# Performance work log

Hardware: AMD Instinct MI355X
Metric: run time of the kernel (lower is better)

Reference implementation:

```python
import jax, jax.numpy as jnp
import numpy as np

B_, L_, DM = 64, 2048, 12
DI, DS, DC, DTR = 24, 16, 4, 1  # d_inner=expand*d_model, d_state, d_conv, dt_rank=ceil(12/16)


def _ln(x, g, b, eps=1e-12):
    m = x.mean(-1, keepdims=True)
    v = ((x - m) ** 2).mean(-1, keepdims=True)
    return (x - m) / jnp.sqrt(v + eps) * g + b


def setup_inputs() -> dict:
    key = jax.random.key(0)
    ks = jax.random.split(key, 16)
    r = lambda k, s, sc=0.1: jax.random.normal(k, s, jnp.float32) * sc
    A = jnp.tile(jnp.arange(1, DS + 1, dtype=jnp.float32), (DI, 1))  # standard S4D-real init
    return {
        "x": jax.random.normal(ks[0], (B_, L_, DM), jnp.float32),
        "in_proj_w": r(ks[1], (2 * DI, DM)),
        "conv_w": r(ks[2], (DI, 1, DC)),
        "conv_b": r(ks[3], (DI,)),
        "x_proj_w": r(ks[4], (DTR + 2 * DS, DI)),
        "dt_w": r(ks[5], (DI, DTR)),
        "dt_b": r(ks[6], (DI,)),
        "A_log": jnp.log(A),
        "Dp": r(ks[7], (DI,)) + 1.0,
        "out_proj_w": r(ks[8], (DM, DI)),
        "ln1_g": jnp.ones(DM, jnp.float32), "ln1_b": jnp.zeros(DM, jnp.float32),
        "ffn_w1": r(ks[9], (4 * DM, DM)), "ffn_b1": jnp.zeros(4 * DM, jnp.float32),
        "ffn_w2": r(ks[10], (DM, 4 * DM)), "ffn_b2": jnp.zeros(DM, jnp.float32),
        "ffn_ln_g": jnp.ones(DM, jnp.float32), "ffn_ln_b": jnp.zeros(DM, jnp.float32),
        "cnn_w": r(ks[11], (DM, DM, 3)), "cnn_b": r(ks[12], (DM,)),
        "lin1_w": r(ks[13], (12, 24)), "lin1_b": jnp.zeros(12, jnp.float32),
        "lin2_w": r(ks[14], (20, 12)), "lin2_b": jnp.zeros(20, jnp.float32),
        "lin3_w": r(ks[15], (1, 20)), "lin3_b": jnp.zeros(1, jnp.float32),
    }


def reference(x, in_proj_w, conv_w, conv_b, x_proj_w, dt_w, dt_b, A_log, Dp,
              out_proj_w, ln1_g, ln1_b, ffn_w1, ffn_b1, ffn_w2, ffn_b2,
              ffn_ln_g, ffn_ln_b, cnn_w, cnn_b, lin1_w, lin1_b,
              lin2_w, lin2_b, lin3_w, lin3_b):
    Bsz = x.shape[0]
    # ---- Mamba block ----
    xz = jnp.einsum('bld,ed->ble', x, in_proj_w)            # [B,L,2*DI]
    xi, z = xz[..., :DI], xz[..., DI:]
    xc = jax.lax.conv_general_dilated(
        xi.transpose(0, 2, 1), conv_w, (1,), [(DC - 1, 0)],
        dimension_numbers=('NCH', 'OIH', 'NCH'), feature_group_count=DI)
    xi = jax.nn.silu(xc.transpose(0, 2, 1) + conv_b)        # causal depthwise conv + SiLU
    xdb = jnp.einsum('bld,ed->ble', xi, x_proj_w)           # [B,L,dt_rank+2*DS]
    dt, Bm, Cm = xdb[..., :DTR], xdb[..., DTR:DTR + DS], xdb[..., DTR + DS:]
    delta = jax.nn.softplus(jnp.einsum('blr,dr->bld', dt, dt_w) + dt_b)  # [B,L,DI]
    A = -jnp.exp(A_log)                                     # [DI,DS]
    dA = jnp.exp(delta[..., None] * A)                      # [B,L,DI,DS]
    dBx = delta[..., None] * Bm[:, :, None, :] * xi[..., None]

    def step(h, inp):
        a, bx, c = inp
        h = a * h + bx                                      # [B,DI,DS]
        return h, jnp.einsum('bdn,bn->bd', h, c)

    h0 = jnp.zeros((Bsz, DI, DS), x.dtype)
    _, ys = jax.lax.scan(step, h0, (dA.transpose(1, 0, 2, 3),
                                    dBx.transpose(1, 0, 2, 3),
                                    Cm.transpose(1, 0, 2)))
    y = ys.transpose(1, 0, 2) + xi * Dp                     # skip D*x
    y = y * jax.nn.silu(z)
    m_out = jnp.einsum('ble,de->bld', y, out_proj_w)        # [B,L,DM]
    h = _ln(m_out, ln1_g, ln1_b)                            # num_layers==1: no residual
    # ---- FeedForward (with residual + LN) ----
    ff = jax.nn.gelu(jnp.einsum('bld,ed->ble', h, ffn_w1) + ffn_b1, approximate=False)
    ff = jnp.einsum('ble,de->bld', ff, ffn_w2) + ffn_b2
    x_mamba = _ln(ff + h, ffn_ln_g, ffn_ln_b)
    # ---- FFT magnitude + Conv1d path (padding=1 to keep length L; see notes) ----
    xf = jnp.abs(jnp.fft.fft(x, axis=1)).astype(x.dtype)
    xcnn = jax.lax.conv_general_dilated(
        xf.transpose(0, 2, 1), cnn_w, (1,), [(1, 1)],
        dimension_numbers=('NCH', 'OIH', 'NCH')) + cnn_b[None, :, None]
    xcnn = xcnn.transpose(0, 2, 1)                          # [B,L,12]
    # ---- fusion head ----
    comb = jnp.concatenate([x_mamba, xcnn], axis=-1)        # [B,L,24]
    o = jax.nn.elu(jnp.einsum('ble,de->bld', comb, lin1_w) + lin1_b)
    o = jnp.einsum('bld,ed->ble', o, lin2_w) + lin2_b
    o = jnp.einsum('ble,oe->blo', o, lin3_w) + lin3_b       # [B,L,1]
    return jax.nn.sigmoid(o.mean(axis=1)).squeeze()          # [B]
```

## Files before the change

kernel.cpp:

```cpp
#include <hip/hip_runtime.h>
#include <math.h>

#define B_  64
#define L_  2048
#define DM  12
#define DI  24
#define DS  16
#define DC  4
#define DTR 1
#define T_  (B_ * L_)
#define NCHUNK 128
#define CHUNK  16


__device__ __forceinline__ float siluf(float v)  { return v / (1.0f + __expf(-v)); }
__device__ __forceinline__ float eluf(float v) { return v > 0.0f ? v : __expf(v) - 1.0f; }

__device__ __forceinline__ float fast_erff(float x) {
    const float ax = fabsf(x);
    const float t  = 1.0f / fmaf(0.3275911f, ax, 1.0f);
    float p = fmaf(1.061405429f, t, -1.453152027f);
    p = fmaf(p, t, 1.421413741f);
    p = fmaf(p, t, -0.284496736f);
    p = fmaf(p, t, 0.254829592f);
    p *= t;
    const float r = 1.0f - p * __expf(-ax * ax);
    return copysignf(r, x);
}
__device__ __forceinline__ float geluf(float v) {
    return 0.5f * v * (1.0f + fast_erff(v * 0.70710678118654752440f));
}

__global__ __launch_bounds__(256) void k_proj(
    const float* __restrict__ x, const float* __restrict__ w_in,
    const float* __restrict__ conv_w, const float* __restrict__ conv_b,
    const float* __restrict__ xproj_w,
    float* __restrict__ xi_out, float* __restrict__ zs_out,
    float* __restrict__ dt_out, float* __restrict__ Bm_out,
    float* __restrict__ Cm_out)
{
    __shared__ float s_xi[256 + 3][DI + 1];
    __shared__ float s_st[256 * DI];
    const int tid = threadIdx.x;
    const int b   = blockIdx.x >> 3;
    const int l0  = (blockIdx.x & 7) << 8;
    const int l   = l0 + tid;
    const int t   = b * L_ + l;
    const size_t t0 = (size_t)b * L_ + l0;

    float xv[DM];
    *(float4*)&xv[0] = *(const float4*)&x[t * DM + 0];
    *(float4*)&xv[4] = *(const float4*)&x[t * DM + 4];
    *(float4*)&xv[8] = *(const float4*)&x[t * DM + 8];

    float zsv[DI];
#pragma unroll
    for (int e = 0; e < DI; ++e) {
        float acc = 0.0f, accz = 0.0f;
#pragma unroll
        for (int d = 0; d < DM; ++d) {
            acc  += xv[d] * w_in[e * DM + d];
            accz += xv[d] * w_in[(DI + e) * DM + d];
        }
        s_xi[tid + 3][e] = acc;
        zsv[e] = siluf(accz);
    }
    if (tid < 3) {
        const int lh = l0 - 3 + tid;
        if (lh < 0) {
            for (int e = 0; e < DI; ++e) s_xi[tid][e] = 0.0f;
        } else {
            const int th = b * L_ + lh;
            float xh[DM];
            for (int d = 0; d < DM; ++d) xh[d] = x[th * DM + d];
            for (int e = 0; e < DI; ++e) {
                float acc = 0.0f;
                for (int d = 0; d < DM; ++d) acc += xh[d] * w_in[e * DM + d];
                s_xi[tid][e] = acc;
            }
        }
    }
#pragma unroll
    for (int e = 0; e < DI; ++e) s_st[tid * DI + e] = zsv[e];
    __syncthreads();
    {
        float4* g = (float4*)(zs_out + t0 * DI);
        const float4* s4 = (const float4*)s_st;
#pragma unroll
        for (int k = 0; k < 6; ++k) g[k * 256 + tid] = s4[k * 256 + tid];
    }

    float xi[DI];
#pragma unroll
    for (int dch = 0; dch < DI; ++dch) {
        float acc = conv_b[dch];
#pragma unroll
        for (int k = 0; k < DC; ++k) acc += s_xi[tid + k][dch] * conv_w[dch * DC + k];
        xi[dch] = siluf(acc);
    }
    float dt = 0.0f;
#pragma unroll
    for (int d = 0; d < DI; ++d) dt += xi[d] * xproj_w[d];
    dt_out[t] = dt;
    float Bv[DS], Cv[DS];
#pragma unroll
    for (int e = 0; e < DS; ++e) {
        float accB = 0.0f, accC = 0.0f;
#pragma unroll
        for (int d = 0; d < DI; ++d) {
            accB += xi[d] * xproj_w[(1 + e) * DI + d];
            accC += xi[d] * xproj_w[(1 + DS + e) * DI + d];
        }
        Bv[e] = accB;
        Cv[e] = accC;
    }

    __syncthreads();
#pragma unroll
    for (int e = 0; e < DI; ++e) s_st[tid * DI + e] = xi[e];
    __syncthreads();
    {
        float4* g = (float4*)(xi_out + t0 * DI);
        const float4* s4 = (const float4*)s_st;
#pragma unroll
        for (int k = 0; k < 6; ++k) g[k * 256 + tid] = s4[k * 256 + tid];
    }
    __syncthreads();
#pragma unroll
    for (int e = 0; e < DS; ++e) s_st[tid * DS + e] = Bv[e];
    __syncthreads();
    {
        float4* g = (float4*)(Bm_out + t0 * DS);
        const float4* s4 = (const float4*)s_st;
#pragma unroll
        for (int k = 0; k < 4; ++k) g[k * 256 + tid] = s4[k * 256 + tid];
    }
    __syncthreads();
#pragma unroll
    for (int e = 0; e < DS; ++e) s_st[tid * DS + e] = Cv[e];
    __syncthreads();
    {
        float4* g = (float4*)(Cm_out + t0 * DS);
        const float4* s4 = (const float4*)s_st;
#pragma unroll
        for (int k = 0; k < 4; ++k) g[k * 256 + tid] = s4[k * 256 + tid];
    }
}

__global__ __launch_bounds__(384) void k_scan1(
    const float* __restrict__ dt_in, const float* __restrict__ xi,
    const float* __restrict__ Bm, const float* __restrict__ A_log,
    const float* __restrict__ dt_w, const float* __restrict__ dt_b,
    float* __restrict__ Sd, float* __restrict__ H)
{
    const int tid = threadIdx.x;
    const int d   = tid % DI;
    const int cl  = tid / DI;
    const int b   = blockIdx.x >> 3;
    const int c   = ((blockIdx.x & 7) << 4) + cl;
    const int t0  = b * L_ + c * CHUNK;

    float An[DS];
#pragma unroll
    for (int j = 0; j < DS; ++j) An[j] = -__expf(A_log[d * DS + j]);
    const float dtw = dt_w[d], dtb = dt_b[d];

    float h[DS];
#pragma unroll
    for (int j = 0; j < DS; ++j) h[j] = 0.0f;
    float sumdel = 0.0f;

    const float*  pDt = dt_in + t0;
    const float*  pX  = xi + (size_t)t0 * DI + d;
    const float4* pB  = (const float4*)(Bm + (size_t)t0 * DS);

#pragma unroll 4
    for (int i = 0; i < CHUNK; ++i) {
        const float v = fmaf(pDt[i], dtw, dtb);
        const float e = __expf(v);
        const float delta = (v > 20.0f) ? v : __logf(1.0f + e);
        const float u = delta * pX[i * DI];
        sumdel += delta;
        const float4 B0 = pB[i * 4 + 0];
        const float4 B1 = pB[i * 4 + 1];
        const float4 B2 = pB[i * 4 + 2];
        const float4 B3 = pB[i * 4 + 3];
#pragma unroll
        for (int j = 0; j < DS; ++j) {
            const float a = __expf(delta * An[j]);
            h[j] = a * h[j] + u * ((j < 4) ? (&B0.x)[j] : (j < 8) ? (&B1.x)[j - 4]
                                   : (j < 12) ? (&B2.x)[j - 8] : (&B3.x)[j - 12]);
        }
    }
    const int cu = (b * DI + d) * NCHUNK + c;
    Sd[cu] = sumdel;
    float4* pH = (float4*)(H + (size_t)cu * DS);
    pH[0] = make_float4(h[0], h[1], h[2], h[3]);
    pH[1] = make_float4(h[4], h[5], h[6], h[7]);
    pH[2] = make_float4(h[8], h[9], h[10], h[11]);
    pH[3] = make_float4(h[12], h[13], h[14], h[15]);
}

__global__ __launch_bounds__(256) void k_scan2(
    const float* __restrict__ Sd, float* __restrict__ H,
    const float* __restrict__ A_log)
{
    const int idx  = blockIdx.x * 256 + threadIdx.x;
    const int n    = idx & 15;
    const int rest = idx >> 4;
    const int d    = rest % DI;
    const float An = -__expf(A_log[d * DS + n]);
    float Hc = 0.0f;
    const int base = rest * NCHUNK;
    for (int cg = 0; cg < NCHUNK / 8; ++cg) {
        float sd[8], hh[8];
#pragma unroll
        for (int k = 0; k < 8; ++k) {
            sd[k] = Sd[base + cg * 8 + k];
            hh[k] = H[(base + cg * 8 + k) * DS + n];
        }
        float aa[8];
#pragma unroll
        for (int k = 0; k < 8; ++k) aa[k] = __expf(An * sd[k]);
#pragma unroll
        for (int k = 0; k < 8; ++k) {
            H[(base + cg * 8 + k) * DS + n] = Hc;
            Hc = aa[k] * Hc + hh[k];
        }
    }
}

__global__ __launch_bounds__(384) void k_scan3(
    const float* __restrict__ dt_in, const float* __restrict__ xi,
    const float* __restrict__ Bm, const float* __restrict__ Cm,
    const float* __restrict__ zs, const float* __restrict__ Dp,
    const float* __restrict__ H0, const float* __restrict__ A_log,
    const float* __restrict__ dt_w, const float* __restrict__ dt_b,
    float* __restrict__ y_out)
{
    const int tid = threadIdx.x;
    const int d   = tid % DI;
    const int cl  = tid / DI;
    const int b   = blockIdx.x >> 3;
    const int c   = ((blockIdx.x & 7) << 4) + cl;
    const int t0  = b * L_ + c * CHUNK;

    float An[DS];
#pragma unroll
    for (int j = 0; j < DS; ++j) An[j] = -__expf(A_log[d * DS + j]);
    const float dtw = dt_w[d], dtb = dt_b[d];
    const float Dpd = Dp[d];

    const int cu = (b * DI + d) * NCHUNK + c;
    float h[DS];
    {
        const float4* pH0 = (const float4*)(H0 + (size_t)cu * DS);
        const float4 a0 = pH0[0], a1 = pH0[1], a2 = pH0[2], a3 = pH0[3];
        h[0]=a0.x; h[1]=a0.y; h[2]=a0.z; h[3]=a0.w;
        h[4]=a1.x; h[5]=a1.y; h[6]=a1.z; h[7]=a1.w;
        h[8]=a2.x; h[9]=a2.y; h[10]=a2.z; h[11]=a2.w;
        h[12]=a3.x; h[13]=a3.y; h[14]=a3.z; h[15]=a3.w;
    }

    const float*  pDt = dt_in + t0;
    const float*  pX  = xi + (size_t)t0 * DI + d;
    const float*  pZ  = zs + (size_t)t0 * DI + d;
    const float4* pB  = (const float4*)(Bm + (size_t)t0 * DS);
    const float4* pC  = (const float4*)(Cm + (size_t)t0 * DS);
    float*        pY  = y_out + (size_t)t0 * DI + d;

#pragma unroll 4
    for (int i = 0; i < CHUNK; ++i) {
        const float v = fmaf(pDt[i], dtw, dtb);
        const float e = __expf(v);
        const float delta = (v > 20.0f) ? v : __logf(1.0f + e);
        const float xiv = pX[i * DI];
        const float u = delta * xiv;
        const float4 B0 = pB[i * 4 + 0];
        const float4 B1 = pB[i * 4 + 1];
        const float4 B2 = pB[i * 4 + 2];
        const float4 B3 = pB[i * 4 + 3];
        const float4 C0 = pC[i * 4 + 0];
        const float4 C1 = pC[i * 4 + 1];
        const float4 C2 = pC[i * 4 + 2];
        const float4 C3 = pC[i * 4 + 3];
        float p = 0.0f;
#pragma unroll
        for (int j = 0; j < DS; ++j) {
            const float a = __expf(delta * An[j]);
            const float Bj = (j < 4) ? (&B0.x)[j] : (j < 8) ? (&B1.x)[j - 4]
                             : (j < 12) ? (&B2.x)[j - 8] : (&B3.x)[j - 12];
            const float Cj = (j < 4) ? (&C0.x)[j] : (j < 8) ? (&C1.x)[j - 4]
                             : (j < 12) ? (&C2.x)[j - 8] : (&C3.x)[j - 12];
            h[j] = a * h[j] + u * Bj;
            p += h[j] * Cj;
        }
        pY[i * DI] = (p + xiv * Dpd) * pZ[i * DI];
    }
}

__global__ __launch_bounds__(256) void k_fft(
    const float* __restrict__ x, float* __restrict__ xfT)
{
    __shared__ float re[2048], im[2048], twr[1024], twi[1024];
    const int tid = threadIdx.x;
    const int b   = blockIdx.x / (DM / 2);
    const int p   = blockIdx.x % (DM / 2);
    for (int j = tid; j < 1024; j += 256) {
        const float ang = -6.283185307179586f * (float)j * (1.0f / 2048.0f);
        float s, c;
        sincosf(ang, &s, &c);
        twr[j] = c; twi[j] = s;
    }
    for (int i = tid; i < 2048; i += 256) {
        const int r = (int)(__brev((unsigned)i) >> 21);
        const float2 v = *(const float2*)&x[(size_t)(b * L_ + i) * DM + 2 * p];
        re[r] = v.x;
        im[r] = v.y;
    }
    __syncthreads();
    for (int s = 1; s <= 11; ++s) {
        const int half  = 1 << (s - 1);
        const int tstep = 2048 >> s;
        for (int i = tid; i < 1024; i += 256) {
            const int j   = i & (half - 1);
            const int grp = i >> (s - 1);
            const int pos = (grp << s) + j;
            const float wr = twr[j * tstep], wi = twi[j * tstep];
            const float ar = re[pos + half], ai = im[pos + half];
            const float vr = wr * ar - wi * ai;
            const float vi = wr * ai + wi * ar;
            const float ur = re[pos], ui = im[pos];
            re[pos] = ur + vr;          im[pos] = ui + vi;
            re[pos + half] = ur - vr;   im[pos + half] = ui - vi;
        }
        __syncthreads();
    }
    float* row1 = xfT + (size_t)(b * DM + 2 * p) * L_;
    float* row2 = row1 + L_;
    for (int k = tid; k < 2048; k += 256) {
        const int nk = (2048 - k) & 2047;
        const float zr = re[k],  zi = im[k];
        const float qr = re[nk], qi = im[nk];
        const float e1r = zr + qr, e1i = zi - qi;
        const float e2r = zr - qr, e2i = zi + qi;
        row1[k] = 0.5f * sqrtf(e1r * e1r + e1i * e1i);
        row2[k] = 0.5f * sqrtf(e2r * e2r + e2i * e2i);
    }
}

__global__ __launch_bounds__(256, 2) void k_tail(
    const float* __restrict__ yg, const float* __restrict__ xfT,
    const float* __restrict__ out_w,
    const float* __restrict__ ln1_g, const float* __restrict__ ln1_b,
    const float* __restrict__ w1, const float* __restrict__ b1,
    const float* __restrict__ w2, const float* __restrict__ b2,
    const float* __restrict__ lng, const float* __restrict__ lnb,
    const float* __restrict__ cnn_w, const float* __restrict__ cnn_b,
    const float* __restrict__ l1w, const float* __restrict__ l1b,
    const float* __restrict__ l2w, const float* __restrict__ l2b,
    const float* __restrict__ l3w,
    float* __restrict__ part)
{
    __shared__ float sV[DM];
    __shared__ float sC0;
    __shared__ float sred[256];

    const int tid = threadIdx.x;
    const int b   = blockIdx.x >> 3;
    const int l   = ((blockIdx.x & 7) << 8) + tid;
    const int t   = b * L_ + l;

    float y[DI];
#pragma unroll
    for (int e = 0; e < DI; ++e) y[e] = yg[(size_t)t * DI + e];
    float xfm[DM], xf0[DM], xfp[DM];
#pragma unroll
    for (int i = 0; i < DM; ++i) {
        const float* row = xfT + (size_t)(b * DM + i) * L_;
        xfm[i] = (l == 0)      ? 0.0f : row[l - 1];
        xf0[i] = row[l];
        xfp[i] = (l == L_ - 1) ? 0.0f : row[l + 1];
    }

    if (tid < DM) {
        float acc = 0.0f;
#pragma unroll
        for (int e = 0; e < 20; ++e) acc += l3w[e] * l2w[e * DM + tid];
        sV[tid] = acc;
    }
    if (tid == DM) {
        float c = 0.0f;
#pragma unroll
        for (int e = 0; e < 20; ++e) c += l2b[e] * l3w[e];
        sC0 = c;
    }
    __syncthreads();

    float m[DM];
#pragma unroll
    for (int j = 0; j < DM; ++j) {
        float acc = 0.0f;
#pragma unroll
        for (int e = 0; e < DI; ++e) acc += y[e] * out_w[j * DI + e];
        m[j] = acc;
    }
    float mean = 0.0f;
#pragma unroll
    for (int j = 0; j < DM; ++j) mean += m[j];
    mean *= (1.0f / DM);
    float var = 0.0f;
#pragma unroll
    for (int j = 0; j < DM; ++j) { const float dv = m[j] - mean; var += dv * dv; }
    var *= (1.0f / DM);
    const float inv1 = rsqrtf(var + 1e-12f);
    float h[DM];
#pragma unroll
    for (int j = 0; j < DM; ++j) h[j] = (m[j] - mean) * inv1 * ln1_g[j] + ln1_b[j];

    float ff[4 * DM];
#pragma unroll
    for (int e = 0; e < 4 * DM; ++e) {
        float acc = b1[e];
#pragma unroll
        for (int j = 0; j < DM; ++j) acc += h[j] * w1[e * DM + j];
        ff[e] = geluf(acc);
    }
    float f2[DM];
#pragma unroll
    for (int j = 0; j < DM; ++j) {
        float acc = b2[j];
#pragma unroll
        for (int e = 0; e < 4 * DM; ++e) acc += ff[e] * w2[j * (4 * DM) + e];
        f2[j] = acc + h[j];
    }
    mean = 0.0f;
#pragma unroll
    for (int j = 0; j < DM; ++j) mean += f2[j];
    mean *= (1.0f / DM);
    var = 0.0f;
#pragma unroll
    for (int j = 0; j < DM; ++j) { const float dv = f2[j] - mean; var += dv * dv; }
    var *= (1.0f / DM);
    const float inv2 = rsqrtf(var + 1e-12f);
    float xm[DM];
#pragma unroll
    for (int j = 0; j < DM; ++j) xm[j] = (f2[j] - mean) * inv2 * lng[j] + lnb[j];

    float xc[DM];
#pragma unroll
    for (int o = 0; o < DM; ++o) {
        float acc = cnn_b[o];
#pragma unroll
        for (int i = 0; i < DM; ++i) {
            const int wb = (o * DM + i) * 3;
            acc += xfm[i] * cnn_w[wb] + xf0[i] * cnn_w[wb + 1] + xfp[i] * cnn_w[wb + 2];
        }
        xc[o] = acc;
    }

    float o3 = sC0;
#pragma unroll
    for (int d = 0; d < DM; ++d) {
        float acc = l1b[d];
#pragma unroll
        for (int e = 0; e < DM; ++e) acc += xm[e] * l1w[d * (2 * DM) + e];
#pragma unroll
        for (int e = 0; e < DM; ++e) acc += xc[e] * l1w[d * (2 * DM) + DM + e];
        o3 += eluf(acc) * sV[d];
    }

    sred[tid] = o3;
    __syncthreads();
    for (int s = 128; s > 0; s >>= 1) {
        if (tid < s) sred[tid] += sred[tid + s];
        __syncthreads();
    }
    if (tid == 0) part[blockIdx.x] = sred[0];
}

__global__ void k_final(const float* __restrict__ part, const float* __restrict__ l3b,
                        float* __restrict__ out)
{
    const int b = threadIdx.x;
    if (b < B_) {
        float s = 0.0f;
        for (int i = 0; i < 8; ++i) s += part[b * 8 + i];
        s = s * (1.0f / (float)L_) + l3b[0];
        out[b] = 1.0f / (1.0f + __expf(-s));
    }
}

extern "C" void kernel_launch(void* const* d_in, const int* in_sizes, int n_in,
                              void* d_out, int out_size, void* d_ws, size_t ws_size,
                              hipStream_t stream)
{
    const float* x        = (const float*)d_in[0];
    const float* in_w     = (const float*)d_in[1];
    const float* conv_w   = (const float*)d_in[2];
    const float* conv_b   = (const float*)d_in[3];
    const float* xproj_w  = (const float*)d_in[4];
    const float* dt_w     = (const float*)d_in[5];
    const float* dt_b     = (const float*)d_in[6];
    const float* A_log    = (const float*)d_in[7];
    const float* Dp       = (const float*)d_in[8];
    const float* out_w    = (const float*)d_in[9];
    const float* ln1_g    = (const float*)d_in[10];
    const float* ln1_b    = (const float*)d_in[11];
    const float* ffn_w1   = (const float*)d_in[12];
    const float* ffn_b1   = (const float*)d_in[13];
    const float* ffn_w2   = (const float*)d_in[14];
    const float* ffn_b2   = (const float*)d_in[15];
    const float* ffn_ln_g = (const float*)d_in[16];
    const float* ffn_ln_b = (const float*)d_in[17];
    const float* cnn_w    = (const float*)d_in[18];
    const float* cnn_b    = (const float*)d_in[19];
    const float* l1w      = (const float*)d_in[20];
    const float* l1b      = (const float*)d_in[21];
    const float* l2w      = (const float*)d_in[22];
    const float* l2b      = (const float*)d_in[23];
    const float* l3w      = (const float*)d_in[24];
    const float* l3b      = (const float*)d_in[25];
    float* out = (float*)d_out;

    float* ws = (float*)d_ws;
    const size_t nTDI = (size_t)T_ * DI;
    const size_t nTDS = (size_t)T_ * DS;
    const size_t nCH  = (size_t)B_ * DI * NCHUNK;
    float* w_xi   = ws;
    float* w_zs   = w_xi + nTDI;
    float* w_y    = w_zs + nTDI;
    float* w_dt   = w_y + nTDI;
    float* w_Bm   = w_dt + T_;
    float* w_Cm   = w_Bm + nTDS;
    float* w_Sd   = w_Cm + nTDS;
    float* w_H    = w_Sd + nCH;
    float* w_xf   = w_H + nCH * DS;
    float* w_part = w_xf + (size_t)B_ * DM * L_;

    k_proj<<<512, 256, 0, stream>>>(x, in_w, conv_w, conv_b, xproj_w,
                                    w_xi, w_zs, w_dt, w_Bm, w_Cm);
    k_scan1<<<B_ * (NCHUNK / 16), 384, 0, stream>>>(w_dt, w_xi, w_Bm, A_log,
                                                    dt_w, dt_b, w_Sd, w_H);
    k_scan2<<<96, 256, 0, stream>>>(w_Sd, w_H, A_log);
    k_fft<<<B_ * (DM / 2), 256, 0, stream>>>(x, w_xf);
    k_scan3<<<B_ * (NCHUNK / 16), 384, 0, stream>>>(w_dt, w_xi, w_Bm, w_Cm, w_zs, Dp,
                                                    w_H, A_log, dt_w, dt_b, w_y);
    k_tail<<<512, 256, 0, stream>>>(w_y, w_xf, out_w,
                                    ln1_g, ln1_b, ffn_w1, ffn_b1, ffn_w2, ffn_b2,
                                    ffn_ln_g, ffn_ln_b, cnn_w, cnn_b,
                                    l1w, l1b, l2w, l2b, l3w, w_part);
    k_final<<<1, 64, 0, stream>>>(w_part, l3b, out);
}
```

Measured before the change: 164.3 us.

## Fuse three-pass chunked scan into one kernel and merge FFT into projection

The three scan kernels (local chunk scan, serial carry propagation, rescan) become one kernel where each block owns one (batch, channel) pair and its 128 chunks. Carries are combined with a Hillis-Steele scan in shared memory, which drops the Sd/H global round trip and two launches. The FFT blocks are appended to the projection grid so both run in a single launch and can overlap. The trade-offs are block-wide syncs in the log-step scan, small 128-thread blocks, and a shared smem buffer sized for the larger of the two roles.

After: 293.9 us. +78.9%, slower.

```diff
diff --git a/kernel.cpp b/kernel.cpp
--- a/kernel.cpp
+++ b/kernel.cpp
@@ -31,149 +31,204 @@
     return 0.5f * v * (1.0f + fast_erff(v * 0.70710678118654752440f));
 }
 
-__global__ __launch_bounds__(256) void k_proj(
+__global__ __launch_bounds__(256) void k_proj_fft(
     const float* __restrict__ x, const float* __restrict__ w_in,
     const float* __restrict__ conv_w, const float* __restrict__ conv_b,
     const float* __restrict__ xproj_w,
     float* __restrict__ xi_out, float* __restrict__ zs_out,
     float* __restrict__ dt_out, float* __restrict__ Bm_out,
-    float* __restrict__ Cm_out)
+    float* __restrict__ Cm_out, float* __restrict__ xfT)
 {
-    __shared__ float s_xi[256 + 3][DI + 1];
-    __shared__ float s_st[256 * DI];
+    __shared__ float smem[12620];
     const int tid = threadIdx.x;
-    const int b   = blockIdx.x >> 3;
-    const int l0  = (blockIdx.x & 7) << 8;
-    const int l   = l0 + tid;
-    const int t   = b * L_ + l;
-    const size_t t0 = (size_t)b * L_ + l0;
-
-    float xv[DM];
-    *(float4*)&xv[0] = *(const float4*)&x[t * DM + 0];
-    *(float4*)&xv[4] = *(const float4*)&x[t * DM + 4];
-    *(float4*)&xv[8] = *(const float4*)&x[t * DM + 8];
-
-    float zsv[DI];
-#pragma unroll
-    for (int e = 0; e < DI; ++e) {
-        float acc = 0.0f, accz = 0.0f;
-#pragma unroll
-        for (int d = 0; d < DM; ++d) {
-            acc  += xv[d] * w_in[e * DM + d];
-            accz += xv[d] * w_in[(DI + e) * DM + d];
-        }
-        s_xi[tid + 3][e] = acc;
-        zsv[e] = siluf(accz);
-    }
-    if (tid < 3) {
-        const int lh = l0 - 3 + tid;
-        if (lh < 0) {
-            for (int e = 0; e < DI; ++e) s_xi[tid][e] = 0.0f;
-        } else {
-            const int th = b * L_ + lh;
-            float xh[DM];
-            for (int d = 0; d < DM; ++d) xh[d] = x[th * DM + d];
-            for (int e = 0; e < DI; ++e) {
-                float acc = 0.0f;
-                for (int d = 0; d < DM; ++d) acc += xh[d] * w_in[e * DM + d];
-                s_xi[tid][e] = acc;
+
+    if (blockIdx.x < 512) {
+        float* s_st = smem + 6476;
+        const int b   = blockIdx.x >> 3;
+        const int l0  = (blockIdx.x & 7) << 8;
+        const int l   = l0 + tid;
+        const int t   = b * L_ + l;
+        const size_t t0 = (size_t)b * L_ + l0;
+
+        float xv[DM];
+        *(float4*)&xv[0] = *(const float4*)&x[t * DM + 0];
+        *(float4*)&xv[4] = *(const float4*)&x[t * DM + 4];
+        *(float4*)&xv[8] = *(const float4*)&x[t * DM + 8];
+
+        float zsv[DI];
+#pragma unroll
+        for (int e = 0; e < DI; ++e) {
+            float acc = 0.0f, accz = 0.0f;
+#pragma unroll
+            for (int d = 0; d < DM; ++d) {
+                acc  += xv[d] * w_in[e * DM + d];
+                accz += xv[d] * w_in[(DI + e) * DM + d];
             }
-        }
-    }
-#pragma unroll
-    for (int e = 0; e < DI; ++e) s_st[tid * DI + e] = zsv[e];
-    __syncthreads();
-    {
-        float4* g = (float4*)(zs_out + t0 * DI);
-        const float4* s4 = (const float4*)s_st;
-#pragma unroll
-        for (int k = 0; k < 6; ++k) g[k * 256 + tid] = s4[k * 256 + tid];
-    }
-
-    float xi[DI];
-#pragma unroll
-    for (int dch = 0; dch < DI; ++dch) {
-        float acc = conv_b[dch];
-#pragma unroll
-        for (int k = 0; k < DC; ++k) acc += s_xi[tid + k][dch] * conv_w[dch * DC + k];
-        xi[dch] = siluf(acc);
-    }
-    float dt = 0.0f;
-#pragma unroll
-    for (int d = 0; d < DI; ++d) dt += xi[d] * xproj_w[d];
-    dt_out[t] = dt;
-    float Bv[DS], Cv[DS];
-#pragma unroll
-    for (int e = 0; e < DS; ++e) {
-        float accB = 0.0f, accC = 0.0f;
-#pragma unroll
-        for (int d = 0; d < DI; ++d) {
-            accB += xi[d] * xproj_w[(1 + e) * DI + d];
-            accC += xi[d] * xproj_w[(1 + DS + e) * DI + d];
-        }
-        Bv[e] = accB;
-        Cv[e] = accC;
-    }
-
-    __syncthreads();
-#pragma unroll
-    for (int e = 0; e < DI; ++e) s_st[tid * DI + e] = xi[e];
-    __syncthreads();
-    {
-        float4* g = (float4*)(xi_out + t0 * DI);
-        const float4* s4 = (const float4*)s_st;
-#pragma unroll
-        for (int k = 0; k < 6; ++k) g[k * 256 + tid] = s4[k * 256 + tid];
-    }
-    __syncthreads();
-#pragma unroll
-    for (int e = 0; e < DS; ++e) s_st[tid * DS + e] = Bv[e];
-    __syncthreads();
-    {
-        float4* g = (float4*)(Bm_out + t0 * DS);
-        const float4* s4 = (const float4*)s_st;
-#pragma unroll
-        for (int k = 0; k < 4; ++k) g[k * 256 + tid] = s4[k * 256 + tid];
-    }
-    __syncthreads();
-#pragma unroll
-    for (int e = 0; e < DS; ++e) s_st[tid * DS + e] = Cv[e];
-    __syncthreads();
-    {
-        float4* g = (float4*)(Cm_out + t0 * DS);
-        const float4* s4 = (const float4*)s_st;
-#pragma unroll
-        for (int k = 0; k < 4; ++k) g[k * 256 + tid] = s4[k * 256 + tid];
-    }
-}
-
-__global__ __launch_bounds__(384) void k_scan1(
+            smem[(tid + 3) * 25 + e] = acc;
+            zsv[e] = siluf(accz);
+        }
+        if (tid < 3) {
+            const int lh = l0 - 3 + tid;
+            if (lh < 0) {
+                for (int e = 0; e < DI; ++e) smem[tid * 25 + e] = 0.0f;
+            } else {
+                const int th = b * L_ + lh;
+                float xh[DM];
+                for (int d = 0; d < DM; ++d) xh[d] = x[th * DM + d];
+                for (int e = 0; e < DI; ++e) {
+                    float acc = 0.0f;
+                    for (int d = 0; d < DM; ++d) acc += xh[d] * w_in[e * DM + d];
+                    smem[tid * 25 + e] = acc;
+                }
+            }
+        }
+#pragma unroll
+        for (int e = 0; e < DI; ++e) s_st[tid * DI + e] = zsv[e];
+        __syncthreads();
+        {
+            float4* g = (float4*)(zs_out + t0 * DI);
+            const float4* s4 = (const float4*)s_st;
+#pragma unroll
+            for (int k = 0; k < 6; ++k) g[k * 256 + tid] = s4[k * 256 + tid];
+        }
+
+        float xi[DI];
+#pragma unroll
+        for (int dch = 0; dch < DI; ++dch) {
+            float acc = conv_b[dch];
+#pragma unroll
+            for (int k = 0; k < DC; ++k)
+                acc += smem[(tid + k) * 25 + dch] * conv_w[dch * DC + k];
+            xi[dch] = siluf(acc);
+        }
+        float dt = 0.0f;
+#pragma unroll
+        for (int d = 0; d < DI; ++d) dt += xi[d] * xproj_w[d];
+        dt_out[t] = dt;
+        float Bv[DS], Cv[DS];
+#pragma unroll
+        for (int e = 0; e < DS; ++e) {
+            float accB = 0.0f, accC = 0.0f;
+#pragma unroll
+            for (int d = 0; d < DI; ++d) {
+                accB += xi[d] * xproj_w[(1 + e) * DI + d];
+                accC += xi[d] * xproj_w[(1 + DS + e) * DI + d];
+            }
+            Bv[e] = accB;
+            Cv[e] = accC;
+        }
+
+        __syncthreads();
+#pragma unroll
+        for (int e = 0; e < DI; ++e) s_st[tid * DI + e] = xi[e];
+        __syncthreads();
+        {
+            float4* g = (float4*)(xi_out + t0 * DI);
+            const float4* s4 = (const float4*)s_st;
+#pragma unroll
+            for (int k = 0; k < 6; ++k) g[k * 256 + tid] = s4[k * 256 + tid];
+        }
+        __syncthreads();
+#pragma unroll
+        for (int e = 0; e < DS; ++e) s_st[tid * DS + e] = Bv[e];
+        __syncthreads();
+        {
+            float4* g = (float4*)(Bm_out + t0 * DS);
+            const float4* s4 = (const float4*)s_st;
+#pragma unroll
+            for (int k = 0; k < 4; ++k) g[k * 256 + tid] = s4[k * 256 + tid];
+        }
+        __syncthreads();
+#pragma unroll
+        for (int e = 0; e < DS; ++e) s_st[tid * DS + e] = Cv[e];
+        __syncthreads();
+        {
+            float4* g = (float4*)(Cm_out + t0 * DS);
+            const float4* s4 = (const float4*)s_st;
+#pragma unroll
+            for (int k = 0; k < 4; ++k) g[k * 256 + tid] = s4[k * 256 + tid];
+        }
+    } else {
+        float* re  = smem;
+        float* im  = smem + 2048;
+        float* twr = smem + 4096;
+        float* twi = smem + 5120;
+        const int bid = blockIdx.x - 512;
+        const int b   = bid / (DM / 2);
+        const int p   = bid % (DM / 2);
+        for (int j = tid; j < 1024; j += 256) {
+            const float ang = -6.283185307179586f * (float)j * (1.0f / 2048.0f);
+            float s, c;
+            sincosf(ang, &s, &c);
+            twr[j] = c; twi[j] = s;
+        }
+        for (int i = tid; i < 2048; i += 256) {
+            const int r = (int)(__brev((unsigned)i) >> 21);
+            const float2 v = *(const float2*)&x[(size_t)(b * L_ + i) * DM + 2 * p];
+            re[r] = v.x;
+            im[r] = v.y;
+        }
+        __syncthreads();
+        for (int s = 1; s <= 11; ++s) {
+            const int half  = 1 << (s - 1);
+            const int tstep = 2048 >> s;
+            for (int i = tid; i < 1024; i += 256) {
+                const int j   = i & (half - 1);
+                const int grp = i >> (s - 1);
+                const int pos = (grp << s) + j;
+                const float wr = twr[j * tstep], wi = twi[j * tstep];
+                const float ar = re[pos + half], ai = im[pos + half];
+                const float vr = wr * ar - wi * ai;
+                const float vi = wr * ai + wi * ar;
+                const float ur = re[pos], ui = im[pos];
+                re[pos] = ur + vr;          im[pos] = ui + vi;
+                re[pos + half] = ur - vr;   im[pos + half] = ui - vi;
+            }
+            __syncthreads();
+        }
+        float* row1 = xfT + (size_t)(b * DM + 2 * p) * L_;
+        float* row2 = row1 + L_;
+        for (int k = tid; k < 2048; k += 256) {
+            const int nk = (2048 - k) & 2047;
+            const float zr = re[k],  zi = im[k];
+            const float qr = re[nk], qi = im[nk];
+            const float e1r = zr + qr, e1i = zi - qi;
+            const float e2r = zr - qr, e2i = zi + qi;
+            row1[k] = 0.5f * sqrtf(e1r * e1r + e1i * e1i);
+            row2[k] = 0.5f * sqrtf(e2r * e2r + e2i * e2i);
+        }
+    }
+}
+
+__global__ __launch_bounds__(128) void k_scan(
     const float* __restrict__ dt_in, const float* __restrict__ xi,
-    const float* __restrict__ Bm, const float* __restrict__ A_log,
+    const float* __restrict__ Bm, const float* __restrict__ Cm,
+    const float* __restrict__ zs, const float* __restrict__ Dp,
+    const float* __restrict__ A_log,
     const float* __restrict__ dt_w, const float* __restrict__ dt_b,
-    float* __restrict__ Sd, float* __restrict__ H)
+    float* __restrict__ y_out)
 {
-    const int tid = threadIdx.x;
-    const int d   = tid % DI;
-    const int cl  = tid / DI;
-    const int b   = blockIdx.x >> 3;
-    const int c   = ((blockIdx.x & 7) << 4) + cl;
-    const int t0  = b * L_ + c * CHUNK;
+    __shared__ float sA[NCHUNK][17];
+    __shared__ float sH[NCHUNK][17];
+    const int c = threadIdx.x;
+    const int b = blockIdx.x / DI;
+    const int d = blockIdx.x % DI;
+    const int t0 = b * L_ + c * CHUNK;
 
     float An[DS];
 #pragma unroll
     for (int j = 0; j < DS; ++j) An[j] = -__expf(A_log[d * DS + j]);
     const float dtw = dt_w[d], dtb = dt_b[d];
-
-    float h[DS];
-#pragma unroll
-    for (int j = 0; j < DS; ++j) h[j] = 0.0f;
-    float sumdel = 0.0f;
+    const float Dpd = Dp[d];
 
     const float*  pDt = dt_in + t0;
     const float*  pX  = xi + (size_t)t0 * DI + d;
     const float4* pB  = (const float4*)(Bm + (size_t)t0 * DS);
 
+    float h[DS];
+#pragma unroll
+    for (int j = 0; j < DS; ++j) h[j] = 0.0f;
+    float sumdel = 0.0f;
 #pragma unroll 4
     for (int i = 0; i < CHUNK; ++i) {
         const float v = fmaf(pDt[i], dtw, dtb);
@@ -192,83 +247,38 @@
                                    : (j < 12) ? (&B2.x)[j - 8] : (&B3.x)[j - 12]);
         }
     }
-    const int cu = (b * DI + d) * NCHUNK + c;
-    Sd[cu] = sumdel;
-    float4* pH = (float4*)(H + (size_t)cu * DS);
-    pH[0] = make_float4(h[0], h[1], h[2], h[3]);
-    pH[1] = make_float4(h[4], h[5], h[6], h[7]);
-    pH[2] = make_float4(h[8], h[9], h[10], h[11]);
-    pH[3] = make_float4(h[12], h[13], h[14], h[15]);
-}
-
-__global__ __launch_bounds__(256) void k_scan2(
-    const float* __restrict__ Sd, float* __restrict__ H,
-    const float* __restrict__ A_log)
-{
-    const int idx  = blockIdx.x * 256 + threadIdx.x;
-    const int n    = idx & 15;
-    const int rest = idx >> 4;
-    const int d    = rest % DI;
-    const float An = -__expf(A_log[d * DS + n]);
-    float Hc = 0.0f;
-    const int base = rest * NCHUNK;
-    for (int cg = 0; cg < NCHUNK / 8; ++cg) {
-        float sd[8], hh[8];
-#pragma unroll
-        for (int k = 0; k < 8; ++k) {
-            sd[k] = Sd[base + cg * 8 + k];
-            hh[k] = H[(base + cg * 8 + k) * DS + n];
-        }
-        float aa[8];
-#pragma unroll
-        for (int k = 0; k < 8; ++k) aa[k] = __expf(An * sd[k]);
-#pragma unroll
-        for (int k = 0; k < 8; ++k) {
-            H[(base + cg * 8 + k) * DS + n] = Hc;
-            Hc = aa[k] * Hc + hh[k];
-        }
-    }
-}
-
-__global__ __launch_bounds__(384) void k_scan3(
-    const float* __restrict__ dt_in, const float* __restrict__ xi,
-    const float* __restrict__ Bm, const float* __restrict__ Cm,
-    const float* __restrict__ zs, const float* __restrict__ Dp,
-    const float* __restrict__ H0, const float* __restrict__ A_log,
-    const float* __restrict__ dt_w, const float* __restrict__ dt_b,
-    float* __restrict__ y_out)
-{
-    const int tid = threadIdx.x;
-    const int d   = tid % DI;
-    const int cl  = tid / DI;
-    const int b   = blockIdx.x >> 3;
-    const int c   = ((blockIdx.x & 7) << 4) + cl;
-    const int t0  = b * L_ + c * CHUNK;
-
-    float An[DS];
-#pragma unroll
-    for (int j = 0; j < DS; ++j) An[j] = -__expf(A_log[d * DS + j]);
-    const float dtw = dt_w[d], dtb = dt_b[d];
-    const float Dpd = Dp[d];
-
-    const int cu = (b * DI + d) * NCHUNK + c;
-    float h[DS];
-    {
-        const float4* pH0 = (const float4*)(H0 + (size_t)cu * DS);
-        const float4 a0 = pH0[0], a1 = pH0[1], a2 = pH0[2], a3 = pH0[3];
-        h[0]=a0.x; h[1]=a0.y; h[2]=a0.z; h[3]=a0.w;
-        h[4]=a1.x; h[5]=a1.y; h[6]=a1.z; h[7]=a1.w;
-        h[8]=a2.x; h[9]=a2.y; h[10]=a2.z; h[11]=a2.w;
-        h[12]=a3.x; h[13]=a3.y; h[14]=a3.z; h[15]=a3.w;
-    }
-
-    const float*  pDt = dt_in + t0;
-    const float*  pX  = xi + (size_t)t0 * DI + d;
-    const float*  pZ  = zs + (size_t)t0 * DI + d;
-    const float4* pB  = (const float4*)(Bm + (size_t)t0 * DS);
-    const float4* pC  = (const float4*)(Cm + (size_t)t0 * DS);
-    float*        pY  = y_out + (size_t)t0 * DI + d;
-
+    float a[DS];
+#pragma unroll
+    for (int j = 0; j < DS; ++j) a[j] = __expf(An[j] * sumdel);
+
+#pragma unroll
+    for (int k = 1; k < NCHUNK; k <<= 1) {
+        __syncthreads();
+#pragma unroll
+        for (int j = 0; j < DS; ++j) { sA[c][j] = a[j]; sH[c][j] = h[j]; }
+        __syncthreads();
+        if (c >= k) {
+            float pa[DS], ph[DS];
+#pragma unroll
+            for (int j = 0; j < DS; ++j) { pa[j] = sA[c - k][j]; ph[j] = sH[c - k][j]; }
+#pragma unroll
+            for (int j = 0; j < DS; ++j) {
+                h[j] = fmaf(a[j], ph[j], h[j]);
+                a[j] *= pa[j];
+            }
+        }
+    }
+    __syncthreads();
+#pragma unroll
+    for (int j = 0; j < DS; ++j) sH[c][j] = h[j];
+    __syncthreads();
+    float hr[DS];
+#pragma unroll
+    for (int j = 0; j < DS; ++j) hr[j] = (c == 0) ? 0.0f : sH[c - 1][j];
+
+    const float*  pZ = zs + (size_t)t0 * DI + d;
+    const float4* pC = (const float4*)(Cm + (size_t)t0 * DS);
+    float*        pY = y_out + (size_t)t0 * DI + d;
 #pragma unroll 4
     for (int i = 0; i < CHUNK; ++i) {
         const float v = fmaf(pDt[i], dtw, dtb);
@@ -287,65 +297,15 @@
         float p = 0.0f;
 #pragma unroll
         for (int j = 0; j < DS; ++j) {
-            const float a = __expf(delta * An[j]);
+            const float aa = __expf(delta * An[j]);
             const float Bj = (j < 4) ? (&B0.x)[j] : (j < 8) ? (&B1.x)[j - 4]
                              : (j < 12) ? (&B2.x)[j - 8] : (&B3.x)[j - 12];
             const float Cj = (j < 4) ? (&C0.x)[j] : (j < 8) ? (&C1.x)[j - 4]
                              : (j < 12) ? (&C2.x)[j - 8] : (&C3.x)[j - 12];
-            h[j] = a * h[j] + u * Bj;
-            p += h[j] * Cj;
+            hr[j] = aa * hr[j] + u * Bj;
+            p += hr[j] * Cj;
         }
         pY[i * DI] = (p + xiv * Dpd) * pZ[i * DI];
-    }
-}
-
-__global__ __launch_bounds__(256) void k_fft(
-    const float* __restrict__ x, float* __restrict__ xfT)
-{
-    __shared__ float re[2048], im[2048], twr[1024], twi[1024];
-    const int tid = threadIdx.x;
-    const int b   = blockIdx.x / (DM / 2);
-    const int p   = blockIdx.x % (DM / 2);
-    for (int j = tid; j < 1024; j += 256) {
-        const float ang = -6.283185307179586f * (float)j * (1.0f / 2048.0f);
-        float s, c;
-        sincosf(ang, &s, &c);
-        twr[j] = c; twi[j] = s;
-    }
-    for (int i = tid; i < 2048; i += 256) {
-        const int r = (int)(__brev((unsigned)i) >> 21);
-        const float2 v = *(const float2*)&x[(size_t)(b * L_ + i) * DM + 2 * p];
-        re[r] = v.x;
-        im[r] = v.y;
-    }
-    __syncthreads();
-    for (int s = 1; s <= 11; ++s) {
-        const int half  = 1 << (s - 1);
-        const int tstep = 2048 >> s;
-        for (int i = tid; i < 1024; i += 256) {
-            const int j   = i & (half - 1);
-            const int grp = i >> (s - 1);
-            const int pos = (grp << s) + j;
-            const float wr = twr[j * tstep], wi = twi[j * tstep];
-            const float ar = re[pos + half], ai = im[pos + half];
-            const float vr = wr * ar - wi * ai;
-            const float vi = wr * ai + wi * ar;
-            const float ur = re[pos], ui = im[pos];
-            re[pos] = ur + vr;          im[pos] = ui + vi;
-            re[pos + half] = ur - vr;   im[pos + half] = ui - vi;
-        }
-        __syncthreads();
-    }
-    float* row1 = xfT + (size_t)(b * DM + 2 * p) * L_;
-    float* row2 = row1 + L_;
-    for (int k = tid; k < 2048; k += 256) {
-        const int nk = (2048 - k) & 2047;
-        const float zr = re[k],  zi = im[k];
-        const float qr = re[nk], qi = im[nk];
-        const float e1r = zr + qr, e1i = zi - qi;
-        const float e2r = zr - qr, e2i = zi + qi;
-        row1[k] = 0.5f * sqrtf(e1r * e1r + e1i * e1i);
-        row2[k] = 0.5f * sqrtf(e2r * e2r + e2i * e2i);
     }
 }
 
@@ -526,26 +486,20 @@
     float* ws = (float*)d_ws;
     const size_t nTDI = (size_t)T_ * DI;
     const size_t nTDS = (size_t)T_ * DS;
-    const size_t nCH  = (size_t)B_ * DI * NCHUNK;
     float* w_xi   = ws;
     float* w_zs   = w_xi + nTDI;
     float* w_y    = w_zs + nTDI;
     float* w_dt   = w_y + nTDI;
     float* w_Bm   = w_dt + T_;
     float* w_Cm   = w_Bm + nTDS;
-    float* w_Sd   = w_Cm + nTDS;
-    float* w_H    = w_Sd + nCH;
-    float* w_xf   = w_H + nCH * DS;
+    float* w_xf   = w_Cm + nTDS;
     float* w_part = w_xf + (size_t)B_ * DM * L_;
 
-    k_proj<<<512, 256, 0, stream>>>(x, in_w, conv_w, conv_b, xproj_w,
-                                    w_xi, w_zs, w_dt, w_Bm, w_Cm);
-    k_scan1<<<B_ * (NCHUNK / 16), 384, 0, stream>>>(w_dt, w_xi, w_Bm, A_log,
-                                                    dt_w, dt_b, w_Sd, w_H);
-    k_scan2<<<96, 256, 0, stream>>>(w_Sd, w_H, A_log);
-    k_fft<<<B_ * (DM / 2), 256, 0, stream>>>(x, w_xf);
-    k_scan3<<<B_ * (NCHUNK / 16), 384, 0, stream>>>(w_dt, w_xi, w_Bm, w_Cm, w_zs, Dp,
-                                                    w_H, A_log, dt_w, dt_b, w_y);
+    k_proj_fft<<<512 + B_ * (DM / 2), 256, 0, stream>>>(
+        x, in_w, conv_w, conv_b, xproj_w,
+        w_xi, w_zs, w_dt, w_Bm, w_Cm, w_xf);
+    k_scan<<<B_ * DI, 128, 0, stream>>>(w_dt, w_xi, w_Bm, w_Cm, w_zs, Dp,
+                                        A_log, dt_w, dt_b, w_y);
     k_tail<<<512, 256, 0, stream>>>(w_y, w_xf, out_w,
                                     ln1_g, ln1_b, ffn_w1, ffn_b1, ffn_w2, ffn_b2,
                                     ffn_ln_g, ffn_ln_b, cnn_w, cnn_b,
```

## Merge projection and FFT kernels into one launch with block-range dispatch

Applied to the files above, without the earlier changes.

The input projection kernel and the FFT-magnitude kernel are combined into a single launch. The first 512 blocks do the projection and the remaining blocks do the per-batch FFT, with the shared memory buffer partitioned between the two roles. This removes one kernel launch and lets the independent FFT work overlap with the projection work on the GPU. In exchange, every block now reserves the larger combined shared memory allocation, which may lower occupancy for the projection blocks.

After: 147.4 us (median of 2 runs). 1.11x faster.

```diff
diff --git a/kernel.cpp b/kernel.cpp
--- a/kernel.cpp
+++ b/kernel.cpp
@@ -31,119 +31,172 @@
     return 0.5f * v * (1.0f + fast_erff(v * 0.70710678118654752440f));
 }
 
-__global__ __launch_bounds__(256) void k_proj(
+__global__ __launch_bounds__(256) void k_proj_fft(
     const float* __restrict__ x, const float* __restrict__ w_in,
     const float* __restrict__ conv_w, const float* __restrict__ conv_b,
     const float* __restrict__ xproj_w,
     float* __restrict__ xi_out, float* __restrict__ zs_out,
     float* __restrict__ dt_out, float* __restrict__ Bm_out,
-    float* __restrict__ Cm_out)
-{
-    __shared__ float s_xi[256 + 3][DI + 1];
-    __shared__ float s_st[256 * DI];
+    float* __restrict__ Cm_out, float* __restrict__ xfT)
+{
+    __shared__ float smem[12620];
     const int tid = threadIdx.x;
-    const int b   = blockIdx.x >> 3;
-    const int l0  = (blockIdx.x & 7) << 8;
-    const int l   = l0 + tid;
-    const int t   = b * L_ + l;
-    const size_t t0 = (size_t)b * L_ + l0;
-
-    float xv[DM];
-    *(float4*)&xv[0] = *(const float4*)&x[t * DM + 0];
-    *(float4*)&xv[4] = *(const float4*)&x[t * DM + 4];
-    *(float4*)&xv[8] = *(const float4*)&x[t * DM + 8];
-
-    float zsv[DI];
-#pragma unroll
-    for (int e = 0; e < DI; ++e) {
-        float acc = 0.0f, accz = 0.0f;
-#pragma unroll
-        for (int d = 0; d < DM; ++d) {
-            acc  += xv[d] * w_in[e * DM + d];
-            accz += xv[d] * w_in[(DI + e) * DM + d];
-        }
-        s_xi[tid + 3][e] = acc;
-        zsv[e] = siluf(accz);
-    }
-    if (tid < 3) {
-        const int lh = l0 - 3 + tid;
-        if (lh < 0) {
-            for (int e = 0; e < DI; ++e) s_xi[tid][e] = 0.0f;
-        } else {
-            const int th = b * L_ + lh;
-            float xh[DM];
-            for (int d = 0; d < DM; ++d) xh[d] = x[th * DM + d];
-            for (int e = 0; e < DI; ++e) {
-                float acc = 0.0f;
-                for (int d = 0; d < DM; ++d) acc += xh[d] * w_in[e * DM + d];
-                s_xi[tid][e] = acc;
+
+    if (blockIdx.x < 512) {
+        float* s_st = smem + 6476;
+        const int b   = blockIdx.x >> 3;
+        const int l0  = (blockIdx.x & 7) << 8;
+        const int l   = l0 + tid;
+        const int t   = b * L_ + l;
+        const size_t t0 = (size_t)b * L_ + l0;
+
+        float xv[DM];
+        *(float4*)&xv[0] = *(const float4*)&x[t * DM + 0];
+        *(float4*)&xv[4] = *(const float4*)&x[t * DM + 4];
+        *(float4*)&xv[8] = *(const float4*)&x[t * DM + 8];
+
+        float zsv[DI];
+#pragma unroll
+        for (int e = 0; e < DI; ++e) {
+            float acc = 0.0f, accz = 0.0f;
+#pragma unroll
+            for (int d = 0; d < DM; ++d) {
+                acc  += xv[d] * w_in[e * DM + d];
+                accz += xv[d] * w_in[(DI + e) * DM + d];
             }
-        }
-    }
-#pragma unroll
-    for (int e = 0; e < DI; ++e) s_st[tid * DI + e] = zsv[e];
-    __syncthreads();
-    {
-        float4* g = (float4*)(zs_out + t0 * DI);
-        const float4* s4 = (const float4*)s_st;
-#pragma unroll
-        for (int k = 0; k < 6; ++k) g[k * 256 + tid] = s4[k * 256 + tid];
-    }
-
-    float xi[DI];
-#pragma unroll
-    for (int dch = 0; dch < DI; ++dch) {
-        float acc = conv_b[dch];
-#pragma unroll
-        for (int k = 0; k < DC; ++k) acc += s_xi[tid + k][dch] * conv_w[dch * DC + k];
-        xi[dch] = siluf(acc);
-    }
-    float dt = 0.0f;
-#pragma unroll
-    for (int d = 0; d < DI; ++d) dt += xi[d] * xproj_w[d];
-    dt_out[t] = dt;
-    float Bv[DS], Cv[DS];
-#pragma unroll
-    for (int e = 0; e < DS; ++e) {
-        float accB = 0.0f, accC = 0.0f;
-#pragma unroll
-        for (int d = 0; d < DI; ++d) {
-            accB += xi[d] * xproj_w[(1 + e) * DI + d];
-            accC += xi[d] * xproj_w[(1 + DS + e) * DI + d];
-        }
-        Bv[e] = accB;
-        Cv[e] = accC;
-    }
-
-    __syncthreads();
-#pragma unroll
-    for (int e = 0; e < DI; ++e) s_st[tid * DI + e] = xi[e];
-    __syncthreads();
-    {
-        float4* g = (float4*)(xi_out + t0 * DI);
-        const float4* s4 = (const float4*)s_st;
-#pragma unroll
-        for (int k = 0; k < 6; ++k) g[k * 256 + tid] = s4[k * 256 + tid];
-    }
-    __syncthreads();
-#pragma unroll
-    for (int e = 0; e < DS; ++e) s_st[tid * DS + e] = Bv[e];
-    __syncthreads();
-    {
-        float4* g = (float4*)(Bm_out + t0 * DS);
-        const float4* s4 = (const float4*)s_st;
-#pragma unroll
-        for (int k = 0; k < 4; ++k) g[k * 256 + tid] = s4[k * 256 + tid];
-    }
-    __syncthreads();
-#pragma unroll
-    for (int e = 0; e < DS; ++e) s_st[tid * DS + e] = Cv[e];
-    __syncthreads();
-    {
-        float4* g = (float4*)(Cm_out + t0 * DS);
-        const float4* s4 = (const float4*)s_st;
-#pragma unroll
-        for (int k = 0; k < 4; ++k) g[k * 256 + tid] = s4[k * 256 + tid];
+            smem[(tid + 3) * 25 + e] = acc;
+            zsv[e] = siluf(accz);
+        }
+        if (tid < 3) {
+            const int lh = l0 - 3 + tid;
+            if (lh < 0) {
+                for (int e = 0; e < DI; ++e) smem[tid * 25 + e] = 0.0f;
+            } else {
+                const int th = b * L_ + lh;
+                float xh[DM];
+                for (int d = 0; d < DM; ++d) xh[d] = x[th * DM + d];
+                for (int e = 0; e < DI; ++e) {
+                    float acc = 0.0f;
+                    for (int d = 0; d < DM; ++d) acc += xh[d] * w_in[e * DM + d];
+                    smem[tid * 25 + e] = acc;
+                }
+            }
+        }
+#pragma unroll
+        for (int e = 0; e < DI; ++e) s_st[tid * DI + e] = zsv[e];
+        __syncthreads();
+        {
+            float4* g = (float4*)(zs_out + t0 * DI);
+            const float4* s4 = (const float4*)s_st;
+#pragma unroll
+            for (int k = 0; k < 6; ++k) g[k * 256 + tid] = s4[k * 256 + tid];
+        }
+
+        float xi[DI];
+#pragma unroll
+        for (int dch = 0; dch < DI; ++dch) {
+            float acc = conv_b[dch];
+#pragma unroll
+            for (int k = 0; k < DC; ++k)
+                acc += smem[(tid + k) * 25 + dch] * conv_w[dch * DC + k];
+            xi[dch] = siluf(acc);
+        }
+        float dt = 0.0f;
+#pragma unroll
+        for (int d = 0; d < DI; ++d) dt += xi[d] * xproj_w[d];
+        dt_out[t] = dt;
+        float Bv[DS], Cv[DS];
+#pragma unroll
+        for (int e = 0; e < DS; ++e) {
+            float accB = 0.0f, accC = 0.0f;
+#pragma unroll
+            for (int d = 0; d < DI; ++d) {
+                accB += xi[d] * xproj_w[(1 + e) * DI + d];
+                accC += xi[d] * xproj_w[(1 + DS + e) * DI + d];
+            }
+            Bv[e] = accB;
+            Cv[e] = accC;
+        }
+
+        __syncthreads();
+#pragma unroll
+        for (int e = 0; e < DI; ++e) s_st[tid * DI + e] = xi[e];
+        __syncthreads();
+        {
+            float4* g = (float4*)(xi_out + t0 * DI);
+            const float4* s4 = (const float4*)s_st;
+#pragma unroll
+            for (int k = 0; k < 6; ++k) g[k * 256 + tid] = s4[k * 256 + tid];
+        }
+        __syncthreads();
+#pragma unroll
+        for (int e = 0; e < DS; ++e) s_st[tid * DS + e] = Bv[e];
+        __syncthreads();
+        {
+            float4* g = (float4*)(Bm_out + t0 * DS);
+            const float4* s4 = (const float4*)s_st;
+#pragma unroll
+            for (int k = 0; k < 4; ++k) g[k * 256 + tid] = s4[k * 256 + tid];
+        }
+        __syncthreads();
+#pragma unroll
+        for (int e = 0; e < DS; ++e) s_st[tid * DS + e] = Cv[e];
+        __syncthreads();
+        {
+            float4* g = (float4*)(Cm_out + t0 * DS);
+            const float4* s4 = (const float4*)s_st;
+#pragma unroll
+            for (int k = 0; k < 4; ++k) g[k * 256 + tid] = s4[k * 256 + tid];
+        }
+    } else {
+        float* re  = smem;
+        float* im  = smem + 2048;
+        float* twr = smem + 4096;
+        float* twi = smem + 5120;
+        const int bid = blockIdx.x - 512;
+        const int b   = bid / (DM / 2);
+        const int p   = bid % (DM / 2);
+        for (int j = tid; j < 1024; j += 256) {
+            const float ang = -6.283185307179586f * (float)j * (1.0f / 2048.0f);
+            float s, c;
+            sincosf(ang, &s, &c);
+            twr[j] = c; twi[j] = s;
+        }
+        for (int i = tid; i < 2048; i += 256) {
+            const int r = (int)(__brev((unsigned)i) >> 21);
+            const float2 v = *(const float2*)&x[(size_t)(b * L_ + i) * DM + 2 * p];
+            re[r] = v.x;
+            im[r] = v.y;
+        }
+        __syncthreads();
+        for (int s = 1; s <= 11; ++s) {
+            const int half  = 1 << (s - 1);
+            const int tstep = 2048 >> s;
+            for (int i = tid; i < 1024; i += 256) {
+                const int j   = i & (half - 1);
+                const int grp = i >> (s - 1);
+                const int pos = (grp << s) + j;
+                const float wr = twr[j * tstep], wi = twi[j * tstep];
+                const float ar = re[pos + half], ai = im[pos + half];
+                const float vr = wr * ar - wi * ai;
+                const float vi = wr * ai + wi * ar;
+                const float ur = re[pos], ui = im[pos];
+                re[pos] = ur + vr;          im[pos] = ui + vi;
+                re[pos + half] = ur - vr;   im[pos + half] = ui - vi;
+            }
+            __syncthreads();
+        }
+        float* row1 = xfT + (size_t)(b * DM + 2 * p) * L_;
+        float* row2 = row1 + L_;
+        for (int k = tid; k < 2048; k += 256) {
+            const int nk = (2048 - k) & 2047;
+            const float zr = re[k],  zi = im[k];
+            const float qr = re[nk], qi = im[nk];
+            const float e1r = zr + qr, e1i = zi - qi;
+            const float e2r = zr - qr, e2i = zi + qi;
+            row1[k] = 0.5f * sqrtf(e1r * e1r + e1i * e1i);
+            row2[k] = 0.5f * sqrtf(e2r * e2r + e2i * e2i);
+        }
     }
 }
 
@@ -296,56 +349,6 @@
             p += h[j] * Cj;
         }
         pY[i * DI] = (p + xiv * Dpd) * pZ[i * DI];
-    }
-}
-
-__global__ __launch_bounds__(256) void k_fft(
-    const float* __restrict__ x, float* __restrict__ xfT)
-{
-    __shared__ float re[2048], im[2048], twr[1024], twi[1024];
-    const int tid = threadIdx.x;
-    const int b   = blockIdx.x / (DM / 2);
-    const int p   = blockIdx.x % (DM / 2);
-    for (int j = tid; j < 1024; j += 256) {
-        const float ang = -6.283185307179586f * (float)j * (1.0f / 2048.0f);
-        float s, c;
-        sincosf(ang, &s, &c);
-        twr[j] = c; twi[j] = s;
-    }
-    for (int i = tid; i < 2048; i += 256) {
-        const int r = (int)(__brev((unsigned)i) >> 21);
-        const float2 v = *(const float2*)&x[(size_t)(b * L_ + i) * DM + 2 * p];
-        re[r] = v.x;
-        im[r] = v.y;
-    }
-    __syncthreads();
-    for (int s = 1; s <= 11; ++s) {
-        const int half  = 1 << (s - 1);
-        const int tstep = 2048 >> s;
-        for (int i = tid; i < 1024; i += 256) {
-            const int j   = i & (half - 1);
-            const int grp = i >> (s - 1);
-            const int pos = (grp << s) + j;
-            const float wr = twr[j * tstep], wi = twi[j * tstep];
-            const float ar = re[pos + half], ai = im[pos + half];
-            const float vr = wr * ar - wi * ai;
-            const float vi = wr * ai + wi * ar;
-            const float ur = re[pos], ui = im[pos];
-            re[pos] = ur + vr;          im[pos] = ui + vi;
-            re[pos + half] = ur - vr;   im[pos + half] = ui - vi;
-        }
-        __syncthreads();
-    }
-    float* row1 = xfT + (size_t)(b * DM + 2 * p) * L_;
-    float* row2 = row1 + L_;
-    for (int k = tid; k < 2048; k += 256) {
-        const int nk = (2048 - k) & 2047;
-        const float zr = re[k],  zi = im[k];
-        const float qr = re[nk], qi = im[nk];
-        const float e1r = zr + qr, e1i = zi - qi;
-        const float e2r = zr - qr, e2i = zi + qi;
-        row1[k] = 0.5f * sqrtf(e1r * e1r + e1i * e1i);
-        row2[k] = 0.5f * sqrtf(e2r * e2r + e2i * e2i);
     }
 }
 
@@ -538,12 +541,12 @@
     float* w_xf   = w_H + nCH * DS;
     float* w_part = w_xf + (size_t)B_ * DM * L_;
 
-    k_proj<<<512, 256, 0, stream>>>(x, in_w, conv_w, conv_b, xproj_w,
-                                    w_xi, w_zs, w_dt, w_Bm, w_Cm);
+    k_proj_fft<<<512 + B_ * (DM / 2), 256, 0, stream>>>(
+        x, in_w, conv_w, conv_b, xproj_w,
+        w_xi, w_zs, w_dt, w_Bm, w_Cm, w_xf);
     k_scan1<<<B_ * (NCHUNK / 16), 384, 0, stream>>>(w_dt, w_xi, w_Bm, A_log,
                                                     dt_w, dt_b, w_Sd, w_H);
     k_scan2<<<96, 256, 0, stream>>>(w_Sd, w_H, A_log);
-    k_fft<<<B_ * (DM / 2), 256, 0, stream>>>(x, w_xf);
     k_scan3<<<B_ * (NCHUNK / 16), 384, 0, stream>>>(w_dt, w_xi, w_Bm, w_Cm, w_zs, Dp,
                                                     w_H, A_log, dt_w, dt_b, w_y);
     k_tail<<<512, 256, 0, stream>>>(w_y, w_xf, out_w,
```
